# Optimization experiments

Hardware: AMD Instinct MI355X
Metric: run time of the kernel (lower is better)

The kernel has to match this reference:

```python
import jax, jax.numpy as jnp
import numpy as np

B, T, D = 8, 1024, 1024
H = 16
ATT_DIM = 1024
VAL_DIM = 1024
SCALE = float((D // H) ** 0.5)  # note: uses input_dim//num_heads, not head dim of attention_dim
EPS = 1e-13


def setup_inputs() -> dict:
    key = jax.random.key(0)
    ks = jax.random.split(key, 6)
    inputs = jax.random.normal(ks[0], (B, T, D), dtype=jnp.float32)
    mask = jnp.ones((B, T), dtype=jnp.float32)
    adj = jax.random.uniform(ks[1], (B, T, T), dtype=jnp.float32)
    # combined QKV projection: Linear(D, 2*ATT_DIM + VAL_DIM)
    W_qkv = jax.random.normal(ks[2], (2 * ATT_DIM + VAL_DIM, D), dtype=jnp.float32) * (1.0 / np.sqrt(D))
    b_qkv = jnp.zeros((2 * ATT_DIM + VAL_DIM,), dtype=jnp.float32)
    # output projection: Linear(VAL_DIM, D)
    W_out = jax.random.normal(ks[3], (D, VAL_DIM), dtype=jnp.float32) * (1.0 / np.sqrt(VAL_DIM))
    b_out = jnp.zeros((D,), dtype=jnp.float32)
    return {"inputs": inputs, "mask": mask, "adj": adj,
            "W_qkv": W_qkv, "b_qkv": b_qkv, "W_out": W_out, "b_out": b_out}


def reference(inputs, mask, adj, W_qkv, b_qkv, W_out, b_out):
    b, t, _ = inputs.shape
    dh_a = ATT_DIM // H
    dh_v = VAL_DIM // H
    proj = jnp.einsum('btd,od->bto', inputs, W_qkv) + b_qkv
    q = proj[..., :ATT_DIM]
    k = proj[..., ATT_DIM:2 * ATT_DIM]
    v = proj[..., 2 * ATT_DIM:]
    # [B, H, T, dh]
    q = q.reshape(b, t, H, dh_a).transpose(0, 2, 1, 3)
    k = k.reshape(b, t, H, dh_a).transpose(0, 2, 1, 3)
    v = v.reshape(b, t, H, dh_v).transpose(0, 2, 1, 3)
    scores = jnp.einsum('bhqd,bhkd->bhqk', q, k) / SCALE
    # multiplicative adjacency gate, broadcast over heads
    scores = scores * adj[:, None, :, :]
    # old-allennlp masked_softmax: softmax(scores * mask), re-mask, renormalize
    m = mask[:, None, None, :]  # [B,1,1,T]
    attn = jax.nn.softmax(scores * m, axis=-1)
    attn = attn * m
    attn = attn / (attn.sum(axis=-1, keepdims=True) + EPS)
    out = jnp.einsum('bhqk,bhkd->bhqd', attn, v)  # [B,H,T,dh_v]
    out = out.transpose(0, 2, 1, 3).reshape(b, t, VAL_DIM)
    out = jnp.einsum('btv,ov->bto', out, W_out) + b_out
    return out
```

## Files before the change

### kernel.cpp

```cpp
#include <hip/hip_runtime.h>
#include <hip/hip_bf16.h>
#include <cstdint>


using bf16 = __hip_bfloat16;
typedef __attribute__((ext_vector_type(8))) short short8;
typedef __attribute__((ext_vector_type(4))) short short4v;
typedef __attribute__((ext_vector_type(4))) float floatx4;

#define B_    8
#define T_    1024
#define D_    1024
#define H_    16
#define PROJW 3072

__device__ __forceinline__ void gl2lds16(const void* g, void* l) {
  __builtin_amdgcn_global_load_lds(
      (const __attribute__((address_space(1))) void*)g,
      (__attribute__((address_space(3))) void*)l,
      16, 0, 0);
}

__device__ __forceinline__ unsigned short f2b_bits(float f) {
  return __builtin_bit_cast(unsigned short, __float2bfloat16(f));
}

__global__ __launch_bounds__(256)
void cvt_f32_bf16(const float* __restrict__ src, bf16* __restrict__ dst, int n) {
  int i = (blockIdx.x * 256 + threadIdx.x) * 4;
  if (i < n) {
    floatx4 f = *(const floatx4*)(src + i);
    short4v h;
    h[0] = f2b_bits(f[0]); h[1] = f2b_bits(f[1]);
    h[2] = f2b_bits(f[2]); h[3] = f2b_bits(f[3]);
    *(short4v*)(dst + i) = h;
  }
}

template<int EPI>
__global__ __launch_bounds__(256)
void gemm_bt_bias(const bf16* __restrict__ A, const bf16* __restrict__ Bm,
                  const bf16* __restrict__ bias, void* __restrict__ C0,
                  void* __restrict__ C1, void* __restrict__ C2,
                  int M, int N, int K)
{
  __shared__ __align__(16) unsigned short sA[128 * 64];
  __shared__ __align__(16) unsigned short sB[128 * 64];

  const int tid  = threadIdx.x;
  const int lane = tid & 63;
  const int wv   = tid >> 6;
  const int quad = lane >> 4;
  const int l16  = lane & 15;
  const int wm   = wv >> 1, wn = wv & 1;
  const int bn   = blockIdx.x, bm = blockIdx.y;

  floatx4 acc[4][4];
#pragma unroll
  for (int i = 0; i < 4; ++i)
#pragma unroll
    for (int j = 0; j < 4; ++j) acc[i][j] = (floatx4){0.f, 0.f, 0.f, 0.f};

  const int o_base = wv * 1024 + lane * 16;

  for (int kt = 0; kt < K; kt += 64) {
    __syncthreads();
#pragma unroll
    for (int it = 0; it < 4; ++it) {
      int o = it * 4096 + o_base;
      int row = o >> 7, col = (o & 127) >> 1;
      gl2lds16(A + (size_t)(bm * 128 + row) * K + kt + col,
               &sA[(it * 4096 + wv * 1024) >> 1]);
    }
#pragma unroll
    for (int it = 0; it < 4; ++it) {
      int o = it * 4096 + o_base;
      int row = o >> 7, col = (o & 127) >> 1;
      gl2lds16(Bm + (size_t)(bn * 128 + row) * K + kt + col,
               &sB[(it * 4096 + wv * 1024) >> 1]);
    }
    __syncthreads();

#pragma unroll
    for (int kk = 0; kk < 64; kk += 32) {
      short8 a_[4], b_[4];
#pragma unroll
      for (int i = 0; i < 4; ++i)
        a_[i] = *(const short8*)&sA[(wm * 64 + i * 16 + l16) * 64 + kk + quad * 8];
#pragma unroll
      for (int j = 0; j < 4; ++j)
        b_[j] = *(const short8*)&sB[(wn * 64 + j * 16 + l16) * 64 + kk + quad * 8];
#pragma unroll
      for (int i = 0; i < 4; ++i)
#pragma unroll
        for (int j = 0; j < 4; ++j)
          acc[i][j] = __builtin_amdgcn_mfma_f32_16x16x32_bf16(a_[i], b_[j], acc[i][j], 0, 0, 0);
    }
  }

  if (EPI == 1) {
#pragma unroll
    for (int j = 0; j < 4; ++j) {
      const int colg = bn * 128 + wn * 64 + j * 16 + l16;
      const float bv = __bfloat162float(bias[colg]);
#pragma unroll
      for (int i = 0; i < 4; ++i)
#pragma unroll
        for (int r = 0; r < 4; ++r) {
          int rowg = bm * 128 + wm * 64 + i * 16 + quad * 4 + r;
          ((float*)C0)[(size_t)rowg * N + colg] = acc[i][j][r] + bv;
        }
    }
  } else {
    const int region = bn >> 3;
    if (region < 2) {
      bf16* dst = (bf16*)(region == 0 ? C0 : C1);
#pragma unroll
      for (int j = 0; j < 4; ++j) {
        const int colg = bn * 128 + wn * 64 + j * 16 + l16;
        const int colr = colg & 1023;
        const float bv = __bfloat162float(bias[colg]);
#pragma unroll
        for (int i = 0; i < 4; ++i)
#pragma unroll
          for (int r = 0; r < 4; ++r) {
            int rowg = bm * 128 + wm * 64 + i * 16 + quad * 4 + r;
            dst[(size_t)rowg * 1024 + colr] = __float2bfloat16(acc[i][j][r] + bv);
          }
      }
    } else {
      bf16* vt = (bf16*)C2;
#pragma unroll
      for (int j = 0; j < 4; ++j) {
        const int colg = bn * 128 + wn * 64 + j * 16 + l16;
        const int d  = colg & 63;
        const int hh = (colg >> 6) & 15;
        const float bv = __bfloat162float(bias[colg]);
#pragma unroll
        for (int i = 0; i < 4; ++i) {
          int rowg0 = bm * 128 + wm * 64 + i * 16 + quad * 4;
          int bb = rowg0 >> 10, t0 = rowg0 & 1023;
          short4v pk;
#pragma unroll
          for (int r = 0; r < 4; ++r) pk[r] = (short)f2b_bits(acc[i][j][r] + bv);
          *(short4v*)&vt[((size_t)(bb * 16 + hh) << 16) + ((size_t)d << 10) + t0] = pk;
        }
      }
    }
  }
}

__global__ __launch_bounds__(256)
void attn_fused(const bf16* __restrict__ Qp, const bf16* __restrict__ Kp,
                const bf16* __restrict__ Vt, const float* __restrict__ adj,
                const float* __restrict__ mask, bf16* __restrict__ aout)
{
  __shared__ __align__(16) unsigned short sK[64 * 72];
  __shared__ __align__(16) unsigned short sVT[64 * 72];
  __shared__ __align__(16) unsigned short sP[64 * 72];

  const int tid  = threadIdx.x;
  const int lane = tid & 63;
  const int wv   = tid >> 6;
  const int quad = lane >> 4;
  const int l16  = lane & 15;
  const int h = blockIdx.x, qt = blockIdx.y, b = blockIdx.z;

  const bf16* qbase = Qp + (size_t)(b * T_ + qt * 64 + wv * 16 + l16) * 1024 + h * 64 + quad * 8;
  const short8 aq0 = *(const short8*)qbase;
  const short8 aq1 = *(const short8*)(qbase + 32);

  const int srow0 = tid >> 3;
  const int srow1 = srow0 + 32;
  const int chunk = (tid & 7) * 8;
  const int sig0 = ((srow0 & 15) << 2) | (srow0 >> 4);
  const int sig1 = ((srow1 & 15) << 2) | (srow1 >> 4);
  const bf16* kb0 = Kp + (size_t)(b * T_ + sig0) * 1024 + h * 64 + chunk;
  const bf16* kb1 = Kp + (size_t)(b * T_ + sig1) * 1024 + h * 64 + chunk;
  const bf16* vb0 = Vt + ((size_t)(b * 16 + h) << 16) + ((size_t)srow0 << 10) + chunk;
  const bf16* vb1 = Vt + ((size_t)(b * 16 + h) << 16) + ((size_t)srow1 << 10) + chunk;

  const float* mb = mask + b * T_ + l16 * 4;
  const float* adjr[4];
#pragma unroll
  for (int r = 0; r < 4; ++r)
    adjr[r] = adj + ((size_t)b * T_ + qt * 64 + wv * 16 + quad * 4 + r) * T_ + l16 * 4;

  short8 kr0 = *(const short8*)kb0;
  short8 kr1 = *(const short8*)kb1;
  short8 vr0 = *(const short8*)vb0;
  short8 vr1 = *(const short8*)vb1;

  floatx4 oacc[4];
#pragma unroll
  for (int d = 0; d < 4; ++d) oacc[d] = (floatx4){0.f, 0.f, 0.f, 0.f};
  float L[4] = {0.f, 0.f, 0.f, 0.f};

  const float SC = 0.125f * 1.44269504088896f;

  for (int kt = 0; kt < 16; ++kt) {
    floatx4 av[4];
    floatx4 mk4 = *(const floatx4*)(mb + kt * 64);
#pragma unroll
    for (int r = 0; r < 4; ++r) av[r] = *(const floatx4*)(adjr[r] + kt * 64);
    float cj[4], off[4];
#pragma unroll
    for (int j = 0; j < 4; ++j) {
      cj[j]  = mk4[j] * SC;
      off[j] = (mk4[j] == 0.f) ? -1e30f : 0.f;
    }

    __syncthreads();
    *(short8*)&sK [srow0 * 72 + chunk] = kr0;
    *(short8*)&sK [srow1 * 72 + chunk] = kr1;
    *(short8*)&sVT[srow0 * 72 + chunk] = vr0;
    *(short8*)&sVT[srow1 * 72 + chunk] = vr1;
    __syncthreads();

    {
      int nk = kt < 15 ? kt + 1 : 15;
      size_t ko = (size_t)nk << 16;
      int    vo = nk << 6;
      kr0 = *(const short8*)(kb0 + ko);
      kr1 = *(const short8*)(kb1 + ko);
      vr0 = *(const short8*)(vb0 + vo);
      vr1 = *(const short8*)(vb1 + vo);
    }

    floatx4 sacc[4];
#pragma unroll
    for (int j = 0; j < 4; ++j) sacc[j] = (floatx4){0.f, 0.f, 0.f, 0.f};
#pragma unroll
    for (int kk = 0; kk < 64; kk += 32) {
      short8 aq = kk ? aq1 : aq0;
#pragma unroll
      for (int j = 0; j < 4; ++j) {
        short8 bk = *(const short8*)&sK[(j * 16 + l16) * 72 + kk + quad * 8];
        sacc[j] = __builtin_amdgcn_mfma_f32_16x16x32_bf16(aq, bk, sacc[j], 0, 0, 0);
      }
    }

#pragma unroll
    for (int r = 0; r < 4; ++r) {
      short4v ph;
#pragma unroll
      for (int j = 0; j < 4; ++j) {
        float t = sacc[j][r] * av[r][j];
        float z = fminf(fmaf(t, cj[j], off[j]), 100.f);
        float p = exp2f(z);
        L[r] += p;
        unsigned bits = __builtin_bit_cast(unsigned, p);
        ph[j] = (short)((bits + 0x8000u) >> 16);
      }
      *(short4v*)&sP[(wv * 16 + quad * 4 + r) * 72 + l16 * 4] = ph;
    }

    __asm__ __volatile__("" ::: "memory");

#pragma unroll
    for (int kk = 0; kk < 64; kk += 32) {
      short8 ap = *(const short8*)&sP[(wv * 16 + l16) * 72 + kk + quad * 8];
#pragma unroll
      for (int d = 0; d < 4; ++d) {
        short8 bv = *(const short8*)&sVT[(d * 16 + l16) * 72 + kk + quad * 8];
        oacc[d] = __builtin_amdgcn_mfma_f32_16x16x32_bf16(ap, bv, oacc[d], 0, 0, 0);
      }
    }
  }

#pragma unroll
  for (int r = 0; r < 4; ++r) {
#pragma unroll
    for (int off = 1; off < 16; off <<= 1)
      L[r] += __shfl_xor(L[r], off, 64);
  }
#pragma unroll
  for (int d = 0; d < 4; ++d) {
#pragma unroll
    for (int r = 0; r < 4; ++r) {
      int qrow = qt * 64 + wv * 16 + quad * 4 + r;
      float val = oacc[d][r] / (L[r] + 1e-13f);
      aout[(size_t)(b * T_ + qrow) * 1024 + h * 64 + d * 16 + l16] = __float2bfloat16(val);
    }
  }
}

extern "C" void kernel_launch(void* const* d_in, const int* in_sizes, int n_in,
                              void* d_out, int out_size, void* d_ws, size_t ws_size,
                              hipStream_t stream) {
  const float* inputs = (const float*)d_in[0];
  const float* mask   = (const float*)d_in[1];
  const float* adj    = (const float*)d_in[2];
  const float* W_qkv  = (const float*)d_in[3];
  const float* b_qkv  = (const float*)d_in[4];
  const float* W_out  = (const float*)d_in[5];
  const float* b_out  = (const float*)d_in[6];

  const size_t SEG = (size_t)8192 * 1024;
  bf16* Qp   = (bf16*)d_ws;
  bf16* Kp   = Qp + SEG;
  bf16* Vt   = Kp + SEG;
  bf16* aout = Vt + SEG;
  bf16* wo_bf = Qp;
  bf16* bo_bf = Qp + (size_t)1024 * 1024;

  bf16* ib_bf = (bf16*)d_out;
  bf16* wq_bf = ib_bf + SEG;
  bf16* bq_bf = wq_bf + (size_t)3072 * 1024;

  dim3 blk(256);
  cvt_f32_bf16<<<dim3(8192 * 1024 / 4 / 256), blk, 0, stream>>>(inputs, ib_bf, 8192 * 1024);
  cvt_f32_bf16<<<dim3(3072 * 1024 / 4 / 256), blk, 0, stream>>>(W_qkv, wq_bf, 3072 * 1024);
  cvt_f32_bf16<<<dim3(3), blk, 0, stream>>>(b_qkv, bq_bf, 3072);
  gemm_bt_bias<2><<<dim3(PROJW / 128, (B_ * T_) / 128), blk, 0, stream>>>(
      ib_bf, wq_bf, bq_bf, Qp, Kp, Vt, B_ * T_, PROJW, D_);
  attn_fused<<<dim3(H_, T_ / 64, B_), blk, 0, stream>>>(Qp, Kp, Vt, adj, mask, aout);
  cvt_f32_bf16<<<dim3(1024 * 1024 / 4 / 256), blk, 0, stream>>>(W_out, wo_bf, 1024 * 1024);
  cvt_f32_bf16<<<dim3(1), blk, 0, stream>>>(b_out, bo_bf, 1024);
  gemm_bt_bias<1><<<dim3(D_ / 128, (B_ * T_) / 128), blk, 0, stream>>>(
      aout, wo_bf, bo_bf, d_out, nullptr, nullptr, B_ * T_, D_, D_);
}
```

Measured before the change: 315.2 us.

## Double attention query tile to 128 rows and compute row sums via MFMA

The attention kernel now runs 8 waves per block over 128 query rows, so each K/V tile staged in LDS is reused by twice as many queries and each thread loads half as much. The softmax denominator is accumulated with an extra MFMA against a vector of ones on the bf16-rounded probabilities instead of scalar adds and a final shuffle reduction. s_setprio is raised around the MFMA sections. The trade is fewer blocks in the grid, more LDS per block, and a denominator built from the rounded P values rather than fp32 ones.

```diff
diff --git a/kernel.cpp b/kernel.cpp
--- a/kernel.cpp
+++ b/kernel.cpp
@@ -150,14 +150,14 @@
   }
 }
 
-__global__ __launch_bounds__(256)
+__global__ __launch_bounds__(512)
 void attn_fused(const bf16* __restrict__ Qp, const bf16* __restrict__ Kp,
                 const bf16* __restrict__ Vt, const float* __restrict__ adj,
                 const float* __restrict__ mask, bf16* __restrict__ aout)
 {
   __shared__ __align__(16) unsigned short sK[64 * 72];
   __shared__ __align__(16) unsigned short sVT[64 * 72];
-  __shared__ __align__(16) unsigned short sP[64 * 72];
+  __shared__ __align__(16) unsigned short sP[128 * 72];
 
   const int tid  = threadIdx.x;
   const int lane = tid & 63;
@@ -166,35 +166,33 @@
   const int l16  = lane & 15;
   const int h = blockIdx.x, qt = blockIdx.y, b = blockIdx.z;
 
-  const bf16* qbase = Qp + (size_t)(b * T_ + qt * 64 + wv * 16 + l16) * 1024 + h * 64 + quad * 8;
+  const bf16* qbase = Qp + (size_t)(b * T_ + qt * 128 + wv * 16 + l16) * 1024 + h * 64 + quad * 8;
   const short8 aq0 = *(const short8*)qbase;
   const short8 aq1 = *(const short8*)(qbase + 32);
 
-  const int srow0 = tid >> 3;
-  const int srow1 = srow0 + 32;
+  const int srow  = tid >> 3;
   const int chunk = (tid & 7) * 8;
-  const int sig0 = ((srow0 & 15) << 2) | (srow0 >> 4);
-  const int sig1 = ((srow1 & 15) << 2) | (srow1 >> 4);
-  const bf16* kb0 = Kp + (size_t)(b * T_ + sig0) * 1024 + h * 64 + chunk;
-  const bf16* kb1 = Kp + (size_t)(b * T_ + sig1) * 1024 + h * 64 + chunk;
-  const bf16* vb0 = Vt + ((size_t)(b * 16 + h) << 16) + ((size_t)srow0 << 10) + chunk;
-  const bf16* vb1 = Vt + ((size_t)(b * 16 + h) << 16) + ((size_t)srow1 << 10) + chunk;
+  const int sig = ((srow & 15) << 2) | (srow >> 4);
+  const bf16* kb = Kp + (size_t)(b * T_ + sig) * 1024 + h * 64 + chunk;
+  const bf16* vb = Vt + ((size_t)(b * 16 + h) << 16) + ((size_t)srow << 10) + chunk;
 
   const float* mb = mask + b * T_ + l16 * 4;
   const float* adjr[4];
 #pragma unroll
   for (int r = 0; r < 4; ++r)
-    adjr[r] = adj + ((size_t)b * T_ + qt * 64 + wv * 16 + quad * 4 + r) * T_ + l16 * 4;
-
-  short8 kr0 = *(const short8*)kb0;
-  short8 kr1 = *(const short8*)kb1;
-  short8 vr0 = *(const short8*)vb0;
-  short8 vr1 = *(const short8*)vb1;
+    adjr[r] = adj + ((size_t)b * T_ + qt * 128 + wv * 16 + quad * 4 + r) * T_ + l16 * 4;
+
+  short8 kr = *(const short8*)kb;
+  short8 vr = *(const short8*)vb;
+
+  short8 ones8;
+#pragma unroll
+  for (int i = 0; i < 8; ++i) ones8[i] = (short)0x3F80;
 
   floatx4 oacc[4];
 #pragma unroll
   for (int d = 0; d < 4; ++d) oacc[d] = (floatx4){0.f, 0.f, 0.f, 0.f};
-  float L[4] = {0.f, 0.f, 0.f, 0.f};
+  floatx4 Lacc = (floatx4){0.f, 0.f, 0.f, 0.f};
 
   const float SC = 0.125f * 1.44269504088896f;
 
@@ -211,25 +209,20 @@
     }
 
     __syncthreads();
-    *(short8*)&sK [srow0 * 72 + chunk] = kr0;
-    *(short8*)&sK [srow1 * 72 + chunk] = kr1;
-    *(short8*)&sVT[srow0 * 72 + chunk] = vr0;
-    *(short8*)&sVT[srow1 * 72 + chunk] = vr1;
+    *(short8*)&sK [srow * 72 + chunk] = kr;
+    *(short8*)&sVT[srow * 72 + chunk] = vr;
     __syncthreads();
 
     {
       int nk = kt < 15 ? kt + 1 : 15;
-      size_t ko = (size_t)nk << 16;
-      int    vo = nk << 6;
-      kr0 = *(const short8*)(kb0 + ko);
-      kr1 = *(const short8*)(kb1 + ko);
-      vr0 = *(const short8*)(vb0 + vo);
-      vr1 = *(const short8*)(vb1 + vo);
+      kr = *(const short8*)(kb + ((size_t)nk << 16));
+      vr = *(const short8*)(vb + (nk << 6));
     }
 
     floatx4 sacc[4];
 #pragma unroll
     for (int j = 0; j < 4; ++j) sacc[j] = (floatx4){0.f, 0.f, 0.f, 0.f};
+    __builtin_amdgcn_s_setprio(1);
 #pragma unroll
     for (int kk = 0; kk < 64; kk += 32) {
       short8 aq = kk ? aq1 : aq0;
@@ -239,6 +232,7 @@
         sacc[j] = __builtin_amdgcn_mfma_f32_16x16x32_bf16(aq, bk, sacc[j], 0, 0, 0);
       }
     }
+    __builtin_amdgcn_s_setprio(0);
 
 #pragma unroll
     for (int r = 0; r < 4; ++r) {
@@ -248,7 +242,6 @@
         float t = sacc[j][r] * av[r][j];
         float z = fminf(fmaf(t, cj[j], off[j]), 100.f);
         float p = exp2f(z);
-        L[r] += p;
         unsigned bits = __builtin_bit_cast(unsigned, p);
         ph[j] = (short)((bits + 0x8000u) >> 16);
       }
@@ -257,29 +250,26 @@
 
     __asm__ __volatile__("" ::: "memory");
 
+    __builtin_amdgcn_s_setprio(1);
 #pragma unroll
     for (int kk = 0; kk < 64; kk += 32) {
       short8 ap = *(const short8*)&sP[(wv * 16 + l16) * 72 + kk + quad * 8];
+      Lacc = __builtin_amdgcn_mfma_f32_16x16x32_bf16(ap, ones8, Lacc, 0, 0, 0);
 #pragma unroll
       for (int d = 0; d < 4; ++d) {
         short8 bv = *(const short8*)&sVT[(d * 16 + l16) * 72 + kk + quad * 8];
         oacc[d] = __builtin_amdgcn_mfma_f32_16x16x32_bf16(ap, bv, oacc[d], 0, 0, 0);
       }
     }
-  }
-
-#pragma unroll
-  for (int r = 0; r < 4; ++r) {
-#pragma unroll
-    for (int off = 1; off < 16; off <<= 1)
-      L[r] += __shfl_xor(L[r], off, 64);
-  }
+    __builtin_amdgcn_s_setprio(0);
+  }
+
 #pragma unroll
   for (int d = 0; d < 4; ++d) {
 #pragma unroll
     for (int r = 0; r < 4; ++r) {
-      int qrow = qt * 64 + wv * 16 + quad * 4 + r;
-      float val = oacc[d][r] / (L[r] + 1e-13f);
+      int qrow = qt * 128 + wv * 16 + quad * 4 + r;
+      float val = oacc[d][r] / (Lacc[r] + 1e-13f);
       aout[(size_t)(b * T_ + qrow) * 1024 + h * 64 + d * 16 + l16] = __float2bfloat16(val);
     }
   }
@@ -314,7 +304,7 @@
   cvt_f32_bf16<<<dim3(3), blk, 0, stream>>>(b_qkv, bq_bf, 3072);
   gemm_bt_bias<2><<<dim3(PROJW / 128, (B_ * T_) / 128), blk, 0, stream>>>(
       ib_bf, wq_bf, bq_bf, Qp, Kp, Vt, B_ * T_, PROJW, D_);
-  attn_fused<<<dim3(H_, T_ / 64, B_), blk, 0, stream>>>(Qp, Kp, Vt, adj, mask, aout);
+  attn_fused<<<dim3(H_, T_ / 128, B_), dim3(512), 0, stream>>>(Qp, Kp, Vt, adj, mask, aout);
   cvt_f32_bf16<<<dim3(1024 * 1024 / 4 / 256), blk, 0, stream>>>(W_out, wo_bf, 1024 * 1024);
   cvt_f32_bf16<<<dim3(1), blk, 0, stream>>>(b_out, bo_bf, 1024);
   gemm_bt_bias<1><<<dim3(D_ / 128, (B_ * T_) / 128), blk, 0, stream>>>(
```

Measured after the change: 307.5 us. -2.4%, faster.
